# Kernel tuning notes

Hardware: AMD Instinct MI355X
Metric: run time of the kernel (lower is better)

Reference implementation:

```python
import jax, jax.numpy as jnp
import numpy as np

N = 100000   # num nodes
F = 256      # feat_data dim == args.feat_dim (required by concat shapes)
D = 32       # fixed neighbor count per node
B = 8192     # batch of node indices
NEG = 10     # neg_sample_size (hard-coded in module)


def setup_inputs() -> dict:
    key = jax.random.key(0)
    ks = jax.random.split(key, 9)
    feat_data = jax.random.normal(ks[0], (N, F), dtype=jnp.float32)
    # self.feats[i] = [degrees[i]] * feat_dim
    degrees = jax.random.randint(ks[1], (N,), 1, 64).astype(jnp.float32)
    feats = jnp.tile(degrees[:, None], (1, F))
    W1 = jax.random.normal(ks[2], (F, 2 * F), dtype=jnp.float32) * 0.02
    b1 = jnp.zeros((F,), dtype=jnp.float32)
    W2 = jax.random.normal(ks[3], (F, 2 * F), dtype=jnp.float32) * 0.02
    b2 = jnp.zeros((F,), dtype=jnp.float32)
    adj = jax.random.randint(ks[4], (N, D), 0, N)          # adj_lists as fixed-degree matrix
    inputs1 = jax.random.randint(ks[5], (B,), 0, N)
    inputs2 = jax.random.randint(ks[6], (B,), 0, N)
    neg = jax.random.randint(ks[7], (NEG,), 0, N)           # unigram neg samples (passed in for determinism)
    return dict(feat_data=feat_data, feats=feats, W1=W1, b1=b1, W2=W2, b2=b2,
                adj=adj, inputs1=inputs1, inputs2=inputs2, neg=neg)


def _aggregate(feat_data, feats, W1, b1, W2, b2, adj, nodes):
    # aggregator(nodes): for each node, agg_one_hop over its neighbors, summed.
    node_feats = feat_data[nodes]                            # [B, F]
    nb = adj[nodes]                                          # [B, D]
    # agg_one_hop: linear1(concat(feat_data[nb], feats[nb]))
    nb_in = jnp.concatenate([feat_data[nb], feats[nb]], axis=-1)   # [B, D, 2F]
    emb = jnp.einsum('bdk,ok->bdo', nb_in, W1) + b1          # [B, D, F]
    neighbor_emb = emb.sum(axis=1)                           # [B, F] (bias summed D times, as in torch)
    final_in = jnp.concatenate([node_feats, neighbor_emb], axis=-1)  # [B, 2F]
    return final_in @ W2.T + b2                              # [B, F]


def _l2norm(x):
    # F.normalize(x, dim=1), eps=1e-12
    n = jnp.linalg.norm(x, axis=1, keepdims=True)
    return x / jnp.maximum(n, 1e-12)


def reference(feat_data, feats, W1, b1, W2, b2, adj, inputs1, inputs2, neg):
    out1 = _l2norm(_aggregate(feat_data, feats, W1, b1, W2, b2, adj, inputs1))
    out2 = _l2norm(_aggregate(feat_data, feats, W1, b1, W2, b2, adj, inputs2))
    neg_out = _l2norm(_aggregate(feat_data, feats, W1, b1, W2, b2, adj, neg))
    return (out1, out2, neg_out)
```

## Files before the change

### kernel.cpp

```cpp
#include <hip/hip_runtime.h>
#include <hip/hip_bf16.h>

#define FDIM 256
#define K2   512
#define DNB  32
#define NMAX 100000
#define CONVB 2048

typedef __attribute__((ext_vector_type(8))) short bf16x8;
typedef __attribute__((ext_vector_type(4))) float f32x4;
typedef __attribute__((ext_vector_type(4))) unsigned int u32x4;

__device__ __align__(16) unsigned short g_FDb[(size_t)NMAX * FDIM];
__device__ float g_degb[NMAX];
__device__ __align__(16) unsigned short g_Wc[FDIM * K2];
__device__ float g_c2[FDIM];
__device__ float g_c3[FDIM];

__device__ __forceinline__ unsigned short f2bf(float f) {
    __hip_bfloat16 h = __float2bfloat16(f);
    return *reinterpret_cast<unsigned short*>(&h);
}
__device__ __forceinline__ float bf2f(unsigned short u) {
    return __uint_as_float(((unsigned)u) << 16);
}
__device__ __forceinline__ unsigned int pack2(float lo, float hi) {
    return (unsigned int)f2bf(lo) | ((unsigned int)f2bf(hi) << 16);
}

__global__ __launch_bounds__(256) void build_prep(
    const float* __restrict__ fd,
    const float* __restrict__ feats,
    const float* __restrict__ W1,
    const float* __restrict__ W2,
    const float* __restrict__ b1,
    const float* __restrict__ b2,
    float Dmul, int N,
    unsigned short* tab_p, float* deg_p)
{
    unsigned short* tab = tab_p ? tab_p : g_FDb;
    float* deg = deg_p ? deg_p : g_degb;
    int bid = blockIdx.x;
    int tid = threadIdx.x;

    if (bid >= 256) {
        size_t tidg = (size_t)(bid - 256) * 256 + tid;
        size_t nthr = (size_t)CONVB * 256;
        size_t total8 = (size_t)N * (FDIM / 8);
        const f32x4* in4 = (const f32x4*)fd;
        u32x4* out8 = (u32x4*)tab;

        size_t i = tidg;
        for (; i + 3 * nthr < total8; i += 4 * nthr) {
            f32x4 a[4], b[4];
            #pragma unroll
            for (int j = 0; j < 4; ++j) {
                size_t g = i + (size_t)j * nthr;
                a[j] = __builtin_nontemporal_load(in4 + 2 * g);
                b[j] = __builtin_nontemporal_load(in4 + 2 * g + 1);
            }
            #pragma unroll
            for (int j = 0; j < 4; ++j) {
                size_t g = i + (size_t)j * nthr;
                u32x4 o;
                o.x = pack2(a[j].x, a[j].y);
                o.y = pack2(a[j].z, a[j].w);
                o.z = pack2(b[j].x, b[j].y);
                o.w = pack2(b[j].z, b[j].w);
                __builtin_nontemporal_store(o, out8 + g);
            }
        }
        for (; i < total8; i += nthr) {
            f32x4 a = __builtin_nontemporal_load(in4 + 2 * i);
            f32x4 b = __builtin_nontemporal_load(in4 + 2 * i + 1);
            u32x4 o;
            o.x = pack2(a.x, a.y);
            o.y = pack2(a.z, a.w);
            o.z = pack2(b.x, b.y);
            o.w = pack2(b.z, b.w);
            __builtin_nontemporal_store(o, out8 + i);
        }
        return;
    }

    __shared__ float w2s[FDIM];
    __shared__ float rv[4], ru[4];
    int o = bid;

    for (size_t n = (size_t)o * 256 + tid; n < (size_t)N; n += 65536)
        deg[n] = feats[n * FDIM];

    w2s[tid] = W2[(size_t)o * K2 + FDIM + tid];
    __syncthreads();

    const float* w1a = W1 + tid;
    const float* w1b = W1 + FDIM + tid;
    float acc0 = 0.f, acc1 = 0.f;
    for (int j = 0; j < FDIM; j += 8) {
        float r0[8], r1[8];
        #pragma unroll
        for (int u = 0; u < 8; ++u) {
            r0[u] = w1a[(size_t)(j + u) * K2];
            r1[u] = w1b[(size_t)(j + u) * K2];
        }
        #pragma unroll
        for (int u = 0; u < 8; ++u) {
            acc0 = fmaf(w2s[j + u], r0[u], acc0);
            acc1 = fmaf(w2s[j + u], r1[u], acc1);
        }
    }
    g_Wc[(size_t)o * K2 + FDIM + tid] = f2bf(acc0);
    g_Wc[(size_t)o * K2 + tid]        = f2bf(W2[(size_t)o * K2 + tid]);

    float v = acc1;
    float u = b1[tid] * w2s[tid];
    #pragma unroll
    for (int s = 32; s; s >>= 1) { v += __shfl_down(v, s); u += __shfl_down(u, s); }
    if ((tid & 63) == 0) { rv[tid >> 6] = v; ru[tid >> 6] = u; }
    __syncthreads();
    if (tid == 0) {
        g_c2[o] = rv[0] + rv[1] + rv[2] + rv[3];
        g_c3[o] = b2[o] + Dmul * (ru[0] + ru[1] + ru[2] + ru[3]);
    }
}

__global__ __launch_bounds__(256, 6) void gg_norm(
    const unsigned short* tab_p, const float* deg_p,
    const int* __restrict__ adj,
    const int* __restrict__ in1, int B1,
    const int* __restrict__ in2, int B2,
    const int* __restrict__ neg, int total,
    float* __restrict__ out)
{
    const unsigned short* tab = tab_p ? tab_p : g_FDb;
    const float* deg = deg_p ? deg_p : g_degb;

    __shared__ __align__(16) char lds[16 * 1024];
    __shared__ float Sdeg[16];

    int tid = threadIdx.x, wave = tid >> 6, lane = tid & 63;
    int base = blockIdx.x * 16;

    #pragma unroll
    for (int i = 0; i < 4; ++i) {
        int row = wave * 4 + i;
        int t = base + row;
        char* rowp = lds + row * 1024;
        int swz = (row & 7) << 4;
        int boff = (lane * 8) ^ swz;
        if (t >= total) {
            ushort4 z = make_ushort4(0, 0, 0, 0);
            *(ushort4*)(rowp + boff) = z;
            *(ushort4*)(rowp + 512 + boff) = z;
            if (lane == 0) Sdeg[row] = 0.f;
            continue;
        }
        int node = (t < B1) ? in1[t] : ((t < B1 + B2) ? in2[t - B1] : neg[t - B1 - B2]);

        int idx = 0; float dg = 0.f;
        if (lane < DNB) {
            idx = adj[(size_t)node * DNB + lane];
            dg = deg[idx];
        }
        #pragma unroll
        for (int s = 16; s; s >>= 1) dg += __shfl_down(dg, s);
        if (lane == 0) Sdeg[row] = dg;

        ushort4 nf = *(const ushort4*)(tab + (size_t)node * FDIM + lane * 4);
        *(ushort4*)(rowp + boff) = nf;

        float a0 = 0.f, a1 = 0.f, a2 = 0.f, a3 = 0.f;
        #pragma unroll
        for (int d = 0; d < DNB; d += 8) {
            ushort4 v[8];
            #pragma unroll
            for (int u = 0; u < 8; ++u) {
                int nb = __shfl(idx, d + u);
                v[u] = *(const ushort4*)(tab + (size_t)nb * FDIM + lane * 4);
            }
            #pragma unroll
            for (int u = 0; u < 8; ++u) {
                a0 += bf2f(v[u].x);
                a1 += bf2f(v[u].y);
                a2 += bf2f(v[u].z);
                a3 += bf2f(v[u].w);
            }
        }
        *(ushort4*)(rowp + 512 + boff) =
            make_ushort4(f2bf(a0), f2bf(a1), f2bf(a2), f2bf(a3));
    }
    __syncthreads();

    int l15 = lane & 15, lg = lane >> 4;
    int swzA = (l15 & 7) << 4;
    f32x4 acc[4];
    #pragma unroll
    for (int nt = 0; nt < 4; ++nt) acc[nt] = (f32x4){0.f, 0.f, 0.f, 0.f};

    const char* pA = lds + (size_t)l15 * 1024;
    const unsigned short* wcB = g_Wc + (size_t)(wave * 64 + l15) * K2 + lg * 8;

    #pragma unroll 4
    for (int kk = 0; kk < K2; kk += 32) {
        int kb = kk * 2 + lg * 16;
        bf16x8 a0 = *(const bf16x8*)(pA + (kb ^ swzA));
        #pragma unroll
        for (int nt = 0; nt < 4; ++nt) {
            bf16x8 b = *(const bf16x8*)(wcB + (size_t)nt * 16 * K2 + kk);
            acc[nt] = __builtin_amdgcn_mfma_f32_16x16x32_bf16(a0, b, acc[nt], 0, 0, 0);
        }
    }
    __syncthreads();

    float* outf = (float*)lds;
    #pragma unroll
    for (int nt = 0; nt < 4; ++nt)
        #pragma unroll
        for (int r = 0; r < 4; ++r) {
            int row = lg * 4 + r;
            int col = wave * 64 + nt * 16 + l15;
            outf[row * 256 + col] = acc[nt][r];
        }
    __syncthreads();

    float4 c2v = *(const float4*)(g_c2 + lane * 4);
    float4 c3v = *(const float4*)(g_c3 + lane * 4);
    #pragma unroll
    for (int r = 0; r < 4; ++r) {
        int row = wave * 4 + r;
        int t = base + row;
        if (t >= total) break;
        float sd = Sdeg[row];
        float4 v = *(float4*)(outf + row * 256 + lane * 4);
        v.x += sd * c2v.x + c3v.x;
        v.y += sd * c2v.y + c3v.y;
        v.z += sd * c2v.z + c3v.z;
        v.w += sd * c2v.w + c3v.w;
        float ss = v.x * v.x + v.y * v.y + v.z * v.z + v.w * v.w;
        #pragma unroll
        for (int s = 32; s; s >>= 1) ss += __shfl_xor(ss, s);
        float inv = 1.0f / fmaxf(sqrtf(ss), 1e-12f);
        v.x *= inv; v.y *= inv; v.z *= inv; v.w *= inv;
        *(float4*)(out + (size_t)t * FDIM + lane * 4) = v;
    }
}

extern "C" void kernel_launch(void* const* d_in, const int* in_sizes, int n_in,
                              void* d_out, int out_size, void* d_ws, size_t ws_size,
                              hipStream_t stream) {
    const float* feat_data = (const float*)d_in[0];
    const float* feats     = (const float*)d_in[1];
    const float* W1        = (const float*)d_in[2];
    const float* b1        = (const float*)d_in[3];
    const float* W2        = (const float*)d_in[4];
    const float* b2        = (const float*)d_in[5];
    const int*   adj       = (const int*)d_in[6];
    const int*   in1       = (const int*)d_in[7];
    const int*   in2       = (const int*)d_in[8];
    const int*   neg       = (const int*)d_in[9];

    int B1 = in_sizes[7];
    int B2 = in_sizes[8];
    int Bn = in_sizes[9];
    int N  = in_sizes[0] / FDIM;
    int D  = in_sizes[6] / N;

    float* out = (float*)d_out;
    int total = B1 + B2 + Bn;

    size_t tab_bytes = (size_t)N * FDIM * 2;
    size_t need = ((tab_bytes + 255) & ~(size_t)255) + (size_t)N * 4;
    bool usews = (ws_size >= need);
    unsigned short* tab = usews ? (unsigned short*)d_ws : nullptr;
    float* deg = usews ? (float*)((char*)d_ws + ((tab_bytes + 255) & ~(size_t)255)) : nullptr;

    build_prep<<<256 + CONVB, 256, 0, stream>>>(feat_data, feats, W1, W2, b1, b2,
                                                (float)D, N, tab, deg);
    gg_norm<<<(total + 15) / 16, 256, 0, stream>>>(tab, deg, adj, in1, B1,
                                                   in2, B2, neg, total, out);
}
```

Baseline: 117.3 us.

## Use 1024-thread blocks with one wave per row in gather-GEMM-norm kernel

The fused gather/matmul/normalize kernel now launches 16 waves per block instead of 4. Each wave gathers exactly one row and computes one 16-column output tile, so the per-wave serial gather loop becomes a single iteration. The aim is more memory-level parallelism for the random neighbor gathers. In exchange, each wave issues only one MFMA chain, the launch bound now allows fewer blocks per CU, and block-wide syncs span more waves.

```diff
diff --git a/kernel.cpp b/kernel.cpp
--- a/kernel.cpp
+++ b/kernel.cpp
@@ -124,7 +124,7 @@
     }
 }
 
-__global__ __launch_bounds__(256, 6) void gg_norm(
+__global__ __launch_bounds__(1024, 2) void gg_norm(
     const unsigned short* tab_p, const float* deg_p,
     const int* __restrict__ adj,
     const int* __restrict__ in1, int B1,
@@ -141,107 +141,98 @@
     int tid = threadIdx.x, wave = tid >> 6, lane = tid & 63;
     int base = blockIdx.x * 16;
 
-    #pragma unroll
-    for (int i = 0; i < 4; ++i) {
-        int row = wave * 4 + i;
+    {
+        int row = wave;
         int t = base + row;
         char* rowp = lds + row * 1024;
-        int swz = (row & 7) << 4;
-        int boff = (lane * 8) ^ swz;
+        int boff = (lane * 8) ^ ((row & 7) << 4);
         if (t >= total) {
             ushort4 z = make_ushort4(0, 0, 0, 0);
             *(ushort4*)(rowp + boff) = z;
             *(ushort4*)(rowp + 512 + boff) = z;
             if (lane == 0) Sdeg[row] = 0.f;
-            continue;
-        }
-        int node = (t < B1) ? in1[t] : ((t < B1 + B2) ? in2[t - B1] : neg[t - B1 - B2]);
-
-        int idx = 0; float dg = 0.f;
-        if (lane < DNB) {
-            idx = adj[(size_t)node * DNB + lane];
-            dg = deg[idx];
-        }
-        #pragma unroll
-        for (int s = 16; s; s >>= 1) dg += __shfl_down(dg, s);
-        if (lane == 0) Sdeg[row] = dg;
-
-        ushort4 nf = *(const ushort4*)(tab + (size_t)node * FDIM + lane * 4);
-        *(ushort4*)(rowp + boff) = nf;
-
-        float a0 = 0.f, a1 = 0.f, a2 = 0.f, a3 = 0.f;
-        #pragma unroll
-        for (int d = 0; d < DNB; d += 8) {
-            ushort4 v[8];
-            #pragma unroll
-            for (int u = 0; u < 8; ++u) {
-                int nb = __shfl(idx, d + u);
-                v[u] = *(const ushort4*)(tab + (size_t)nb * FDIM + lane * 4);
-            }
-            #pragma unroll
-            for (int u = 0; u < 8; ++u) {
-                a0 += bf2f(v[u].x);
-                a1 += bf2f(v[u].y);
-                a2 += bf2f(v[u].z);
-                a3 += bf2f(v[u].w);
-            }
-        }
-        *(ushort4*)(rowp + 512 + boff) =
-            make_ushort4(f2bf(a0), f2bf(a1), f2bf(a2), f2bf(a3));
+        } else {
+            int node = (t < B1) ? in1[t] : ((t < B1 + B2) ? in2[t - B1] : neg[t - B1 - B2]);
+
+            int idx = 0; float dg = 0.f;
+            if (lane < DNB) {
+                idx = adj[(size_t)node * DNB + lane];
+                dg = deg[idx];
+            }
+            #pragma unroll
+            for (int s = 16; s; s >>= 1) dg += __shfl_down(dg, s);
+            if (lane == 0) Sdeg[row] = dg;
+
+            ushort4 nf = *(const ushort4*)(tab + (size_t)node * FDIM + lane * 4);
+            *(ushort4*)(rowp + boff) = nf;
+
+            float a0 = 0.f, a1 = 0.f, a2 = 0.f, a3 = 0.f;
+            #pragma unroll
+            for (int d = 0; d < DNB; d += 8) {
+                ushort4 v[8];
+                #pragma unroll
+                for (int u = 0; u < 8; ++u) {
+                    int nb = __shfl(idx, d + u);
+                    v[u] = *(const ushort4*)(tab + (size_t)nb * FDIM + lane * 4);
+                }
+                #pragma unroll
+                for (int u = 0; u < 8; ++u) {
+                    a0 += bf2f(v[u].x);
+                    a1 += bf2f(v[u].y);
+                    a2 += bf2f(v[u].z);
+                    a3 += bf2f(v[u].w);
+                }
+            }
+            *(ushort4*)(rowp + 512 + boff) =
+                make_ushort4(f2bf(a0), f2bf(a1), f2bf(a2), f2bf(a3));
+        }
     }
     __syncthreads();
 
     int l15 = lane & 15, lg = lane >> 4;
     int swzA = (l15 & 7) << 4;
-    f32x4 acc[4];
-    #pragma unroll
-    for (int nt = 0; nt < 4; ++nt) acc[nt] = (f32x4){0.f, 0.f, 0.f, 0.f};
+    f32x4 acc = (f32x4){0.f, 0.f, 0.f, 0.f};
 
     const char* pA = lds + (size_t)l15 * 1024;
-    const unsigned short* wcB = g_Wc + (size_t)(wave * 64 + l15) * K2 + lg * 8;
-
-    #pragma unroll 4
+    const unsigned short* wcB = g_Wc + (size_t)(wave * 16 + l15) * K2 + lg * 8;
+
+    #pragma unroll 8
     for (int kk = 0; kk < K2; kk += 32) {
         int kb = kk * 2 + lg * 16;
         bf16x8 a0 = *(const bf16x8*)(pA + (kb ^ swzA));
-        #pragma unroll
-        for (int nt = 0; nt < 4; ++nt) {
-            bf16x8 b = *(const bf16x8*)(wcB + (size_t)nt * 16 * K2 + kk);
-            acc[nt] = __builtin_amdgcn_mfma_f32_16x16x32_bf16(a0, b, acc[nt], 0, 0, 0);
-        }
+        bf16x8 b = *(const bf16x8*)(wcB + kk);
+        acc = __builtin_amdgcn_mfma_f32_16x16x32_bf16(a0, b, acc, 0, 0, 0);
     }
     __syncthreads();
 
     float* outf = (float*)lds;
     #pragma unroll
-    for (int nt = 0; nt < 4; ++nt)
-        #pragma unroll
-        for (int r = 0; r < 4; ++r) {
-            int row = lg * 4 + r;
-            int col = wave * 64 + nt * 16 + l15;
-            outf[row * 256 + col] = acc[nt][r];
-        }
-    __syncthreads();
-
-    float4 c2v = *(const float4*)(g_c2 + lane * 4);
-    float4 c3v = *(const float4*)(g_c3 + lane * 4);
-    #pragma unroll
     for (int r = 0; r < 4; ++r) {
-        int row = wave * 4 + r;
+        int row = lg * 4 + r;
+        int col = wave * 16 + l15;
+        outf[row * 256 + col] = acc[r];
+    }
+    __syncthreads();
+
+    {
+        int row = wave;
         int t = base + row;
-        if (t >= total) break;
-        float sd = Sdeg[row];
-        float4 v = *(float4*)(outf + row * 256 + lane * 4);
-        v.x += sd * c2v.x + c3v.x;
-        v.y += sd * c2v.y + c3v.y;
-        v.z += sd * c2v.z + c3v.z;
-        v.w += sd * c2v.w + c3v.w;
-        float ss = v.x * v.x + v.y * v.y + v.z * v.z + v.w * v.w;
-        #pragma unroll
-        for (int s = 32; s; s >>= 1) ss += __shfl_xor(ss, s);
-        float inv = 1.0f / fmaxf(sqrtf(ss), 1e-12f);
-        v.x *= inv; v.y *= inv; v.z *= inv; v.w *= inv;
-        *(float4*)(out + (size_t)t * FDIM + lane * 4) = v;
+        if (t < total) {
+            float4 c2v = *(const float4*)(g_c2 + lane * 4);
+            float4 c3v = *(const float4*)(g_c3 + lane * 4);
+            float sd = Sdeg[row];
+            float4 v = *(float4*)(outf + row * 256 + lane * 4);
+            v.x += sd * c2v.x + c3v.x;
+            v.y += sd * c2v.y + c3v.y;
+            v.z += sd * c2v.z + c3v.z;
+            v.w += sd * c2v.w + c3v.w;
+            float ss = v.x * v.x + v.y * v.y + v.z * v.z + v.w * v.w;
+            #pragma unroll
+            for (int s = 32; s; s >>= 1) ss += __shfl_xor(ss, s);
+            float inv = 1.0f / fmaxf(sqrtf(ss), 1e-12f);
+            v.x *= inv; v.y *= inv; v.z *= inv; v.w *= inv;
+            *(float4*)(out + (size_t)t * FDIM + lane * 4) = v;
+        }
     }
 }
 
@@ -276,6 +267,6 @@
 
     build_prep<<<256 + CONVB, 256, 0, stream>>>(feat_data, feats, W1, W2, b1, b2,
                                                 (float)D, N, tab, deg);
-    gg_norm<<<(total + 15) / 16, 256, 0, stream>>>(tab, deg, adj, in1, B1,
-                                                   in2, B2, neg, total, out);
-}
+    gg_norm<<<(total + 15) / 16, 1024, 0, stream>>>(tab, deg, adj, in1, B1,
+                                                    in2, B2, neg, total, out);
+}
```

After: 116.1 us. About the same (-1.0%).
